# Performance work log

Measured on AMD Instinct MI355X. Metric: run time of the kernel, lower is better.

## Reference

```python
import jax, jax.numpy as jnp
import numpy as np
import math

T = 4096        # block_size / sequence length
E = 2048        # embedding_dim
D = 256         # head_dim


def setup_inputs() -> dict:
    key = jax.random.key(0)
    k_x, k_q, k_k, k_v = jax.random.split(key, 4)
    x = jax.random.normal(k_x, (T, E), dtype=jnp.float32)
    # nn.Linear weights are [out_features, in_features]
    s = 1.0 / math.sqrt(E)
    Wq = jax.random.normal(k_q, (D, E), dtype=jnp.float32) * s
    Wk = jax.random.normal(k_k, (D, E), dtype=jnp.float32) * s
    Wv = jax.random.normal(k_v, (D, E), dtype=jnp.float32) * s
    return {"x": x, "Wq": Wq, "Wk": Wk, "Wv": Wv}


def reference(x, Wq, Wk, Wv):
    # Projections: x @ W.T  (torch Linear, no bias)
    Q = x @ Wq.T            # [T, D]
    K = x @ Wk.T            # [T, D]
    V = x @ Wv.T            # [T, D]
    scale = 1.0 / math.sqrt(Q.shape[-1])
    scores = (Q @ K.T) * scale                      # [T, T]
    causal = jnp.tril(jnp.ones((T, T), dtype=bool))
    scores = jnp.where(causal, scores, jnp.float32(-1e10))
    probs = jax.nn.softmax(scores, axis=-1)         # row softmax (torch legacy dim=1 for 2-D)
    return probs @ V                                # [T, D]
```

## Files before the change

### kernel.cpp

```cpp
#include <hip/hip_runtime.h>
#include <hip/hip_bf16.h>

#define T_DIM 4096
#define E_DIM 2048
#define D_DIM 256
#define NT_SPLIT 5

typedef __attribute__((ext_vector_type(4))) float f32x4;
typedef __attribute__((ext_vector_type(8))) short s16x8;

__device__ __forceinline__ unsigned short f2bf(float f) {
  unsigned int u = __float_as_uint(f);
  unsigned int r = (u + 0x7FFFu + ((u >> 16) & 1u)) >> 16;
  return (unsigned short)r;
}
__device__ __forceinline__ float bf2f(unsigned short h) {
  return __uint_as_float(((unsigned int)h) << 16);
}

__device__ __forceinline__ f32x4 mfma16(s16x8 a, s16x8 b, f32x4 c) {
  return __builtin_amdgcn_mfma_f32_16x16x32_bf16(a, b, c, 0, 0, 0);
}

__device__ __forceinline__ void gload_lds16(const void* g, void* l) {
  __builtin_amdgcn_global_load_lds((const __attribute__((address_space(1))) void*)g,
                                   (__attribute__((address_space(3))) void*)l, 16, 0, 0);
}

__global__ __launch_bounds__(256) void cvt_all(const float* __restrict__ x,
                                               const float* __restrict__ wq,
                                               const float* __restrict__ wk,
                                               const float* __restrict__ wv,
                                               unsigned short* __restrict__ xb,
                                               unsigned short* __restrict__ wb) {
  int blk = blockIdx.x;
  const float* src;
  unsigned short* dst;
  int rel;
  if (blk < 4096)      { src = x;  dst = xb;           rel = blk; }
  else if (blk < 4352) { src = wq; dst = wb;           rel = blk - 4096; }
  else if (blk < 4608) { src = wk; dst = wb + 524288;  rel = blk - 4352; }
  else                 { src = wv; dst = wb + 1048576; rel = blk - 4608; }
  int i = rel * 256 + threadIdx.x;
  float4 a = ((const float4*)src)[i * 2];
  float4 b = ((const float4*)src)[i * 2 + 1];
  uint4 o;
  o.x = (unsigned int)f2bf(a.x) | ((unsigned int)f2bf(a.y) << 16);
  o.y = (unsigned int)f2bf(a.z) | ((unsigned int)f2bf(a.w) << 16);
  o.z = (unsigned int)f2bf(b.x) | ((unsigned int)f2bf(b.y) << 16);
  o.w = (unsigned int)f2bf(b.z) | ((unsigned int)f2bf(b.w) << 16);
  ((uint4*)dst)[i] = o;
}

__global__ __launch_bounds__(256, 3) void qkv_gemm(
    const unsigned short* __restrict__ xb, const unsigned short* __restrict__ wb,
    unsigned short* __restrict__ Qg, unsigned short* __restrict__ Kg,
    unsigned short* __restrict__ Vt) {
  __shared__ __align__(16) unsigned short Al[2][128 * 64];
  __shared__ __align__(16) unsigned short Bl[2][64 * 64];
  int tid = threadIdx.x, wid = tid >> 6, lane = tid & 63;
  int lr = lane & 15, lk = lane >> 4;
  int bi_ = (int)blockIdx.x;
  int xcd = bi_ & 7, kk = bi_ >> 3;
  int mb_ = (kk / 12) * 8 + xcd, nb_ = kk % 12;
  int bm0 = mb_ * 128, bn0 = nb_ * 64;
  int wm = (wid >> 1) * 64, wn = (wid & 1) * 32;

  f32x4 acc[4][2];
#pragma unroll
  for (int m = 0; m < 4; ++m)
#pragma unroll
    for (int n = 0; n < 2; ++n) acc[m][n] = (f32x4){0.f, 0.f, 0.f, 0.f};

#define STAGE_QKV(kt, buf)                                                              \
  {                                                                                     \
    int k0 = (kt)*64;                                                                   \
    _Pragma("unroll") for (int i2 = 0; i2 < 4; ++i2) {                                  \
      int ci = (wid * 4 + i2) * 64 + lane;                                              \
      int row = ci >> 3, cc = ci & 7;                                                   \
      gload_lds16(&xb[(size_t)(bm0 + row) * E_DIM + k0 + ((cc ^ (row & 7)) << 3)],      \
                  &Al[buf][(size_t)(wid * 4 + i2) * 512]);                              \
    }                                                                                   \
    _Pragma("unroll") for (int i2 = 0; i2 < 2; ++i2) {                                  \
      int ci = (wid * 2 + i2) * 64 + lane;                                              \
      int row = ci >> 3, cc = ci & 7;                                                   \
      gload_lds16(&wb[(size_t)(bn0 + row) * E_DIM + k0 + ((cc ^ (row & 7)) << 3)],      \
                  &Bl[buf][(size_t)(wid * 2 + i2) * 512]);                              \
    }                                                                                   \
  }

  STAGE_QKV(0, 0);
  for (int kt = 0; kt < 32; ++kt) {
    int cur = kt & 1;
    __syncthreads();
    if (kt + 1 < 32) STAGE_QKV(kt + 1, cur ^ 1);
    s16x8 af[2][4], bfr[2][2];
#pragma unroll
    for (int c = 0; c < 2; ++c) {
#pragma unroll
      for (int m = 0; m < 4; ++m)
        af[c][m] = *(const s16x8*)&Al[cur][(size_t)(wm + m * 16 + lr) * 64 +
                                           (((c * 4 + lk) ^ (lr & 7)) << 3)];
#pragma unroll
      for (int n = 0; n < 2; ++n)
        bfr[c][n] = *(const s16x8*)&Bl[cur][(size_t)(wn + n * 16 + lr) * 64 +
                                            (((c * 4 + lk) ^ (lr & 7)) << 3)];
    }
#pragma unroll
    for (int c = 0; c < 2; ++c)
#pragma unroll
      for (int m = 0; m < 4; ++m)
#pragma unroll
        for (int n = 0; n < 2; ++n) acc[m][n] = mfma16(af[c][m], bfr[c][n], acc[m][n]);
  }

#pragma unroll
  for (int m = 0; m < 4; ++m) {
    int grow = bm0 + wm + m * 16 + lk * 4;
#pragma unroll
    for (int n = 0; n < 2; ++n) {
      int gcol = bn0 + wn + n * 16 + lr;
      unsigned short h[4];
#pragma unroll
      for (int r = 0; r < 4; ++r) h[r] = f2bf(acc[m][n][r]);
      if (gcol < 256) {
#pragma unroll
        for (int r = 0; r < 4; ++r) Qg[(size_t)(grow + r) * D_DIM + gcol] = h[r];
      } else if (gcol < 512) {
#pragma unroll
        for (int r = 0; r < 4; ++r) Kg[(size_t)(grow + r) * D_DIM + gcol - 256] = h[r];
      } else {
        uint2 w;
        w.x = (unsigned int)h[0] | ((unsigned int)h[1] << 16);
        w.y = (unsigned int)h[2] | ((unsigned int)h[3] << 16);
        *(uint2*)&Vt[(size_t)(gcol - 512) * T_DIM + grow] = w;
      }
    }
  }
#undef STAGE_QKV
}

__global__ __launch_bounds__(256, 2) void attn_kernel(
    const unsigned short* __restrict__ Qg, const unsigned short* __restrict__ Kg,
    const unsigned short* __restrict__ Vt, unsigned short* __restrict__ Opart,
    float* __restrict__ mpart, float* __restrict__ lpart) {
  __shared__ __align__(16) unsigned short Kl[2][32 * 256];
  __shared__ __align__(16) unsigned short Vl[2][256 * 32];
  __shared__ __align__(16) unsigned short Pl[4][32 * 40];

  int b = blockIdx.x;
  int t = 31, s = 0;
  {
    int acc = 0;
#pragma unroll 1
    for (int k = 1; k <= 32; ++k) {
      int c = (4 * k + 4) / 5;
      if (acc + c > b) { t = k - 1; s = b - acc; break; }
      acc += c;
    }
  }
  int nt = 4 * (t + 1) - NT_SPLIT * s;
  if (nt > NT_SPLIT) nt = NT_SPLIT;

  int tid = threadIdx.x, wid = tid >> 6, lane = tid & 63;
  int lr = lane & 15, lk = lane >> 4;
  int q0w = t * 128 + wid * 32;
  unsigned short* pl = &Pl[wid][0];

  s16x8 qf[2][8];
#pragma unroll
  for (int qb = 0; qb < 2; ++qb)
#pragma unroll
    for (int c = 0; c < 8; ++c)
      qf[qb][c] = *(const s16x8*)&Qg[(size_t)(q0w + qb * 16 + lr) * D_DIM + c * 32 + lk * 8];

  float m_run[2] = {-1e30f, -1e30f}, l_run[2] = {0.f, 0.f};
  f32x4 Oa[2][16];
#pragma unroll
  for (int qb = 0; qb < 2; ++qb)
#pragma unroll
    for (int d = 0; d < 16; ++d) Oa[qb][d] = (f32x4){0.f, 0.f, 0.f, 0.f};
  const float scale = 0.0625f;
  int j0 = NT_SPLIT * s;

#define STAGE_KV(j, buf)                                                             \
  {                                                                                  \
    int kv_ = (j)*32;                                                                \
    _Pragma("unroll") for (int i2 = 0; i2 < 4; ++i2) {                               \
      int l = (wid * 4 + i2) * 64 + lane;                                            \
      int row = l >> 5, gcs = l & 31;                                                \
      gload_lds16(&Kg[(size_t)(kv_ + row) * D_DIM + ((gcs ^ (row & 7)) << 3)],       \
                  &Kl[buf][(size_t)(wid * 4 + i2) * 512]);                           \
    }                                                                                \
    _Pragma("unroll") for (int i2 = 0; i2 < 4; ++i2) {                               \
      int l = (wid * 4 + i2) * 64 + lane;                                            \
      int d_ = l >> 2, gs = l & 3;                                                   \
      gload_lds16(&Vt[(size_t)d_ * T_DIM + kv_ + ((gs ^ ((d_ >> 1) & 3)) << 3)],     \
                  &Vl[buf][(size_t)(wid * 4 + i2) * 512]);                           \
    }                                                                                \
  }

  STAGE_KV(j0, 0);
  for (int n = 0; n < nt; ++n) {
    int j = j0 + n, kv = j * 32, cur = n & 1;
    __syncthreads();
    if (n + 1 < nt) STAGE_KV(j + 1, cur ^ 1);
    const unsigned short* kl = &Kl[cur][0];
    const unsigned short* vl = &Vl[cur][0];

    f32x4 sa[2][2];
#pragma unroll
    for (int qb = 0; qb < 2; ++qb)
#pragma unroll
      for (int jb = 0; jb < 2; ++jb) sa[qb][jb] = (f32x4){0.f, 0.f, 0.f, 0.f};
    int sw = lr & 7;
#pragma unroll
    for (int jb = 0; jb < 2; ++jb) {
      int rowbase = (jb * 16 + lr) * 32;
#pragma unroll
      for (int c = 0; c < 8; ++c) {
        s16x8 kf = *(const s16x8*)&kl[(size_t)(rowbase + ((c * 4 + lk) ^ sw)) * 8];
        sa[0][jb] = mfma16(kf, qf[0][c], sa[0][jb]);
        sa[1][jb] = mfma16(kf, qf[1][c], sa[1][jb]);
      }
    }

    bool needmask = (kv + 31 > q0w);
    float alpha_s[2];
#pragma unroll
    for (int qb = 0; qb < 2; ++qb) {
      int myq = q0w + qb * 16 + lr;
      float tmax = -1e30f;
#pragma unroll
      for (int jb = 0; jb < 2; ++jb) {
#pragma unroll
        for (int r = 0; r < 4; ++r) {
          float v = sa[qb][jb][r] * scale;
          if (needmask && (kv + jb * 16 + lk * 4 + r) > myq) v = -1e30f;
          sa[qb][jb][r] = v;
          tmax = fmaxf(tmax, v);
        }
      }
      tmax = fmaxf(tmax, __shfl_xor(tmax, 16));
      tmax = fmaxf(tmax, __shfl_xor(tmax, 32));
      float m_new = fmaxf(fmaxf(m_run[qb], tmax), -1e29f);
      alpha_s[qb] = __expf(m_run[qb] - m_new);
      float psum = 0.f;
#pragma unroll
      for (int jb = 0; jb < 2; ++jb) {
        float p0 = __expf(sa[qb][jb][0] - m_new);
        float p1 = __expf(sa[qb][jb][1] - m_new);
        float p2 = __expf(sa[qb][jb][2] - m_new);
        float p3 = __expf(sa[qb][jb][3] - m_new);
        psum += (p0 + p1) + (p2 + p3);
        uint2 w;
        w.x = (unsigned int)f2bf(p0) | ((unsigned int)f2bf(p1) << 16);
        w.y = (unsigned int)f2bf(p2) | ((unsigned int)f2bf(p3) << 16);
        *(uint2*)&pl[(qb * 16 + lr) * 40 + jb * 16 + lk * 4] = w;
      }
      psum += __shfl_xor(psum, 16);
      psum += __shfl_xor(psum, 32);
      l_run[qb] = l_run[qb] * alpha_s[qb] + psum;
      m_run[qb] = m_new;
    }

    float al[2][4];
#pragma unroll
    for (int qb = 0; qb < 2; ++qb)
#pragma unroll
      for (int r = 0; r < 4; ++r) al[qb][r] = __shfl(alpha_s[qb], lk * 4 + r);
#pragma unroll
    for (int qb = 0; qb < 2; ++qb)
#pragma unroll
      for (int d = 0; d < 16; ++d) {
#pragma unroll
        for (int r = 0; r < 4; ++r) Oa[qb][d][r] *= al[qb][r];
      }

    s16x8 pf0 = *(const s16x8*)&pl[lr * 40 + lk * 8];
    s16x8 pf1 = *(const s16x8*)&pl[(16 + lr) * 40 + lk * 8];
    int vsw = lk ^ ((lr >> 1) & 3);
#pragma unroll
    for (int d = 0; d < 16; ++d) {
      s16x8 vf = *(const s16x8*)&vl[(size_t)((d * 16 + lr) * 4 + vsw) * 8];
      Oa[0][d] = mfma16(pf0, vf, Oa[0][d]);
      Oa[1][d] = mfma16(pf1, vf, Oa[1][d]);
    }
  }

#pragma unroll
  for (int d = 0; d < 16; ++d) {
#pragma unroll
    for (int qb = 0; qb < 2; ++qb) {
      unsigned short h[4];
#pragma unroll
      for (int r = 0; r < 4; ++r) h[r] = f2bf(Oa[qb][d][r]);
      uint2 w;
      w.x = (unsigned int)h[0] | ((unsigned int)h[1] << 16);
      w.y = (unsigned int)h[2] | ((unsigned int)h[3] << 16);
      *(uint2*)&Opart[((size_t)b * 256 + d * 16 + lr) * 128 + wid * 32 + qb * 16 + lk * 4] = w;
    }
  }
  if (lk == 0) {
#pragma unroll
    for (int qb = 0; qb < 2; ++qb) {
      mpart[(size_t)b * 128 + wid * 32 + qb * 16 + lr] = m_run[qb];
      lpart[(size_t)b * 128 + wid * 32 + qb * 16 + lr] = l_run[qb];
    }
  }
#undef STAGE_KV
}

__global__ __launch_bounds__(256) void merge_kernel(const unsigned short* __restrict__ Opart,
                                                    const float* __restrict__ mpart,
                                                    const float* __restrict__ lpart,
                                                    float* __restrict__ out) {
  __shared__ float trans[128 * 65];
  int blk = blockIdx.x;
  int t = blk >> 2, d0 = (blk & 3) * 64, q0 = t * 128;
  int ql = threadIdx.x & 127, dg = threadIdx.x >> 7;
  int base = 0;
#pragma unroll 1
  for (int k = 1; k <= t; ++k) base += (4 * k + 4) / 5;
  int nb = (4 * (t + 1) + 4) / 5;

  float M = -1e30f, den = 0.f;
  for (int p = 0; p < nb; ++p) {
    float mp = mpart[(size_t)(base + p) * 128 + ql];
    float lp = lpart[(size_t)(base + p) * 128 + ql];
    float Mn = fmaxf(M, mp);
    den = den * __expf(M - Mn) + __expf(mp - Mn) * lp;
    M = Mn;
  }
  float inv = 1.0f / den;

  float acc[32];
#pragma unroll
  for (int k = 0; k < 32; ++k) acc[k] = 0.f;
  for (int p = 0; p < nb; ++p) {
    float w = __expf(mpart[(size_t)(base + p) * 128 + ql] - M);
    const unsigned short* op = &Opart[((size_t)(base + p) * 256 + d0 + dg) * 128 + ql];
#pragma unroll
    for (int k = 0; k < 32; ++k) acc[k] += w * bf2f(op[(size_t)(2 * k) * 128]);
  }
#pragma unroll
  for (int k = 0; k < 32; ++k) trans[ql * 65 + dg + 2 * k] = acc[k] * inv;
  __syncthreads();

#pragma unroll
  for (int kk = 0; kk < 32; ++kk) {
    int q = (threadIdx.x >> 6) + 4 * kk;
    int dd = threadIdx.x & 63;
    out[(size_t)(q0 + q) * 256 + d0 + dd] = trans[q * 65 + dd];
  }
}

extern "C" void kernel_launch(void* const* d_in, const int* in_sizes, int n_in,
                              void* d_out, int out_size, void* d_ws, size_t ws_size,
                              hipStream_t stream) {
  const float* x  = (const float*)d_in[0];
  const float* Wq = (const float*)d_in[1];
  const float* Wk = (const float*)d_in[2];
  const float* Wv = (const float*)d_in[3];

  char* ws = (char*)d_ws;
  unsigned short* xb = (unsigned short*)(ws);
  unsigned short* wb = (unsigned short*)(ws + 16777216);
  unsigned short* Qg = (unsigned short*)(ws + 19922944);
  unsigned short* Kg = (unsigned short*)(ws + 22020096);
  unsigned short* Vt = (unsigned short*)(ws + 24117248);
  unsigned short* Opart = (unsigned short*)(ws + 26214400);
  float* mpart = (float*)(ws + 54722560);
  float* lpart = (float*)(ws + 54945280);

  cvt_all<<<4864, 256, 0, stream>>>(x, Wq, Wk, Wv, xb, wb);
  qkv_gemm<<<384, 256, 0, stream>>>(xb, wb, Qg, Kg, Vt);
  attn_kernel<<<435, 256, 0, stream>>>(Qg, Kg, Vt, Opart, mpart, lpart);
  merge_kernel<<<128, 256, 0, stream>>>(Opart, mpart, lpart, (float*)d_out);
}
```

Baseline: 112.6 us.

## Remap attention work items across XCDs and use split barriers with vmcnt waits

The attention block index is remapped so that consecutive blocks land on different XCDs, with work grouped by KV split index, so the blocks sharing the same K/V chunks run on the same XCD and can reuse its L2. The merge kernel is rewritten as a single-pass online softmax over this new partial layout. Both GEMM and attention loops replace __syncthreads with a pair of raw s_barriers around an explicit s_waitcnt vmcnt(8), so the loads just issued for the next tile can stay in flight while the current tile is consumed. The hand-written waitcnt depends on the exact number of outstanding loads, which makes it fragile.

```diff
diff --git a/kernel.cpp b/kernel.cpp
--- a/kernel.cpp
+++ b/kernel.cpp
@@ -5,6 +5,7 @@
 #define E_DIM 2048
 #define D_DIM 256
 #define NT_SPLIT 5
+#define NWORK 435
 
 typedef __attribute__((ext_vector_type(4))) float f32x4;
 typedef __attribute__((ext_vector_type(8))) short s16x8;
@@ -25,6 +26,10 @@
 __device__ __forceinline__ void gload_lds16(const void* g, void* l) {
   __builtin_amdgcn_global_load_lds((const __attribute__((address_space(1))) void*)g,
                                    (__attribute__((address_space(3))) void*)l, 16, 0, 0);
+}
+
+__device__ __forceinline__ int tmin_f(int s) {
+  return s ? ((5 * s - 4) / 4 + 1) : 0;
 }
 
 __global__ __launch_bounds__(256) void cvt_all(const float* __restrict__ x,
@@ -92,8 +97,14 @@
   STAGE_QKV(0, 0);
   for (int kt = 0; kt < 32; ++kt) {
     int cur = kt & 1;
-    __syncthreads();
-    if (kt + 1 < 32) STAGE_QKV(kt + 1, cur ^ 1);
+    __builtin_amdgcn_s_barrier();
+    if (kt + 1 < 32) {
+      STAGE_QKV(kt + 1, cur ^ 1);
+      asm volatile("s_waitcnt vmcnt(8)" ::: "memory");
+    } else {
+      asm volatile("s_waitcnt vmcnt(0)" ::: "memory");
+    }
+    __builtin_amdgcn_s_barrier();
     s16x8 af[2][4], bfr[2][2];
 #pragma unroll
     for (int c = 0; c < 2; ++c) {
@@ -148,15 +159,18 @@
   __shared__ __align__(16) unsigned short Vl[2][256 * 32];
   __shared__ __align__(16) unsigned short Pl[4][32 * 40];
 
-  int b = blockIdx.x;
-  int t = 31, s = 0;
+  int i = (int)blockIdx.x;
+  int c = i & 7, ii = i >> 3;
+  int j = (c < 3) ? (c * 55 + ii) : (3 * 55 + (c - 3) * 54 + ii);
+  int s = 0, t = 0;
   {
-    int acc = 0;
+    int jj = j;
 #pragma unroll 1
-    for (int k = 1; k <= 32; ++k) {
-      int c = (4 * k + 4) / 5;
-      if (acc + c > b) { t = k - 1; s = b - acc; break; }
-      acc += c;
+    for (int ss = 0; ss < 26; ++ss) {
+      int tm = tmin_f(ss);
+      int cnt = 32 - tm;
+      if (jj < cnt) { s = ss; t = tm + jj; break; }
+      jj -= cnt;
     }
   }
   int nt = 4 * (t + 1) - NT_SPLIT * s;
@@ -171,8 +185,8 @@
 #pragma unroll
   for (int qb = 0; qb < 2; ++qb)
 #pragma unroll
-    for (int c = 0; c < 8; ++c)
-      qf[qb][c] = *(const s16x8*)&Qg[(size_t)(q0w + qb * 16 + lr) * D_DIM + c * 32 + lk * 8];
+    for (int cc = 0; cc < 8; ++cc)
+      qf[qb][cc] = *(const s16x8*)&Qg[(size_t)(q0w + qb * 16 + lr) * D_DIM + cc * 32 + lk * 8];
 
   float m_run[2] = {-1e30f, -1e30f}, l_run[2] = {0.f, 0.f};
   f32x4 Oa[2][16];
@@ -183,9 +197,9 @@
   const float scale = 0.0625f;
   int j0 = NT_SPLIT * s;
 
-#define STAGE_KV(j, buf)                                                             \
+#define STAGE_KV(jt, buf)                                                            \
   {                                                                                  \
-    int kv_ = (j)*32;                                                                \
+    int kv_ = (jt)*32;                                                               \
     _Pragma("unroll") for (int i2 = 0; i2 < 4; ++i2) {                               \
       int l = (wid * 4 + i2) * 64 + lane;                                            \
       int row = l >> 5, gcs = l & 31;                                                \
@@ -202,9 +216,15 @@
 
   STAGE_KV(j0, 0);
   for (int n = 0; n < nt; ++n) {
-    int j = j0 + n, kv = j * 32, cur = n & 1;
-    __syncthreads();
-    if (n + 1 < nt) STAGE_KV(j + 1, cur ^ 1);
+    int jt = j0 + n, kv = jt * 32, cur = n & 1;
+    __builtin_amdgcn_s_barrier();
+    if (n + 1 < nt) {
+      STAGE_KV(jt + 1, cur ^ 1);
+      asm volatile("s_waitcnt vmcnt(8)" ::: "memory");
+    } else {
+      asm volatile("s_waitcnt vmcnt(0)" ::: "memory");
+    }
+    __builtin_amdgcn_s_barrier();
     const unsigned short* kl = &Kl[cur][0];
     const unsigned short* vl = &Vl[cur][0];
 
@@ -218,10 +238,10 @@
     for (int jb = 0; jb < 2; ++jb) {
       int rowbase = (jb * 16 + lr) * 32;
 #pragma unroll
-      for (int c = 0; c < 8; ++c) {
-        s16x8 kf = *(const s16x8*)&kl[(size_t)(rowbase + ((c * 4 + lk) ^ sw)) * 8];
-        sa[0][jb] = mfma16(kf, qf[0][c], sa[0][jb]);
-        sa[1][jb] = mfma16(kf, qf[1][c], sa[1][jb]);
+      for (int cc = 0; cc < 8; ++cc) {
+        s16x8 kf = *(const s16x8*)&kl[(size_t)(rowbase + ((cc * 4 + lk) ^ sw)) * 8];
+        sa[0][jb] = mfma16(kf, qf[0][cc], sa[0][jb]);
+        sa[1][jb] = mfma16(kf, qf[1][cc], sa[1][jb]);
       }
     }
 
@@ -298,14 +318,14 @@
       uint2 w;
       w.x = (unsigned int)h[0] | ((unsigned int)h[1] << 16);
       w.y = (unsigned int)h[2] | ((unsigned int)h[3] << 16);
-      *(uint2*)&Opart[((size_t)b * 256 + d * 16 + lr) * 128 + wid * 32 + qb * 16 + lk * 4] = w;
+      *(uint2*)&Opart[((size_t)j * 256 + d * 16 + lr) * 128 + wid * 32 + qb * 16 + lk * 4] = w;
     }
   }
   if (lk == 0) {
 #pragma unroll
     for (int qb = 0; qb < 2; ++qb) {
-      mpart[(size_t)b * 128 + wid * 32 + qb * 16 + lr] = m_run[qb];
-      lpart[(size_t)b * 128 + wid * 32 + qb * 16 + lr] = l_run[qb];
+      mpart[(size_t)j * 128 + wid * 32 + qb * 16 + lr] = m_run[qb];
+      lpart[(size_t)j * 128 + wid * 32 + qb * 16 + lr] = l_run[qb];
     }
   }
 #undef STAGE_KV
@@ -319,30 +339,33 @@
   int blk = blockIdx.x;
   int t = blk >> 2, d0 = (blk & 3) * 64, q0 = t * 128;
   int ql = threadIdx.x & 127, dg = threadIdx.x >> 7;
-  int base = 0;
+
+  float M = -1e30f, den = 0.f;
+  float acc[32];
+#pragma unroll
+  for (int k = 0; k < 32; ++k) acc[k] = 0.f;
+
+  int C = 0;
 #pragma unroll 1
-  for (int k = 1; k <= t; ++k) base += (4 * k + 4) / 5;
-  int nb = (4 * (t + 1) + 4) / 5;
-
-  float M = -1e30f, den = 0.f;
-  for (int p = 0; p < nb; ++p) {
-    float mp = mpart[(size_t)(base + p) * 128 + ql];
-    float lp = lpart[(size_t)(base + p) * 128 + ql];
-    float Mn = fmaxf(M, mp);
-    den = den * __expf(M - Mn) + __expf(mp - Mn) * lp;
-    M = Mn;
+  for (int ss = 0; ss < 26; ++ss) {
+    int tm = tmin_f(ss);
+    int cnt = 32 - tm;
+    if (t >= tm && NT_SPLIT * ss < 4 * (t + 1)) {
+      int p = C + (t - tm);
+      float mp = mpart[(size_t)p * 128 + ql];
+      float lp = lpart[(size_t)p * 128 + ql];
+      float Mn = fmaxf(M, mp);
+      float sc = __expf(M - Mn);
+      float w = __expf(mp - Mn);
+      den = den * sc + w * lp;
+      const unsigned short* op = &Opart[((size_t)p * 256 + d0 + dg) * 128 + ql];
+#pragma unroll
+      for (int k = 0; k < 32; ++k) acc[k] = acc[k] * sc + w * bf2f(op[(size_t)(2 * k) * 128]);
+      M = Mn;
+    }
+    C += cnt;
   }
   float inv = 1.0f / den;
-
-  float acc[32];
-#pragma unroll
-  for (int k = 0; k < 32; ++k) acc[k] = 0.f;
-  for (int p = 0; p < nb; ++p) {
-    float w = __expf(mpart[(size_t)(base + p) * 128 + ql] - M);
-    const unsigned short* op = &Opart[((size_t)(base + p) * 256 + d0 + dg) * 128 + ql];
-#pragma unroll
-    for (int k = 0; k < 32; ++k) acc[k] += w * bf2f(op[(size_t)(2 * k) * 128]);
-  }
 #pragma unroll
   for (int k = 0; k < 32; ++k) trans[ql * 65 + dg + 2 * k] = acc[k] * inv;
   __syncthreads();
@@ -375,6 +398,6 @@
 
   cvt_all<<<4864, 256, 0, stream>>>(x, Wq, Wk, Wv, xb, wb);
   qkv_gemm<<<384, 256, 0, stream>>>(xb, wb, Qg, Kg, Vt);
-  attn_kernel<<<435, 256, 0, stream>>>(Qg, Kg, Vt, Opart, mpart, lpart);
+  attn_kernel<<<NWORK, 256, 0, stream>>>(Qg, Kg, Vt, Opart, mpart, lpart);
   merge_kernel<<<128, 256, 0, stream>>>(Opart, mpart, lpart, (float*)d_out);
 }
```

New measurement: 101.3 us. -10.1%, faster.
